# Kernel optimization log

Hardware: AMD Instinct MI355X
Metric: run time of the kernel (lower is better)

Reference implementation:

```python
import jax, jax.numpy as jnp
import numpy as np


def entmax15(scores, axis):
    """Exact entmax-1.5 (Peters & Martins 2019), sort-based threshold."""
    s = jnp.moveaxis(scores, axis, -1)
    s = (s - jnp.max(s, axis=-1, keepdims=True)) / 2.0
    d = s.shape[-1]
    srt = jnp.sort(s, axis=-1)[..., ::-1]  # descending
    rho = jnp.arange(1, d + 1, dtype=s.dtype)
    mean = jnp.cumsum(srt, axis=-1) / rho
    mean_sq = jnp.cumsum(srt * srt, axis=-1) / rho
    ss = rho * (mean_sq - mean * mean)
    delta = (1.0 - ss) / rho
    tau = mean - jnp.sqrt(jnp.clip(delta, 0.0, None))
    support = jnp.sum((tau <= srt).astype(jnp.int32), axis=-1)  # support size k*
    tau_star = jnp.take_along_axis(tau, (support - 1)[..., None], axis=-1)
    p = jnp.square(jnp.clip(s - tau_star, 0.0, None))
    return jnp.moveaxis(p, -1, axis)


def setup_inputs() -> dict:
    key = jax.random.key(0)
    k0, k1, k2 = jax.random.split(key, 3)
    B, S, H, A = 64, 2048, 512, 128
    lstm_output = jax.random.normal(k0, (B, S, H), dtype=jnp.float32)
    W1 = jax.random.normal(k1, (H, A), dtype=jnp.float32) * (1.0 / np.sqrt(H))
    b1 = jnp.zeros((A,), dtype=jnp.float32)
    W2 = jax.random.normal(k2, (A, 1), dtype=jnp.float32) * (1.0 / np.sqrt(A))
    b2 = jnp.zeros((1,), dtype=jnp.float32)
    return {"lstm_output": lstm_output, "W1": W1, "b1": b1, "W2": W2, "b2": b2}


def reference(lstm_output, W1, b1, W2, b2):
    # score MLP: Linear -> tanh -> Linear, squeeze(-1)
    h = jnp.tanh(lstm_output @ W1 + b1)            # [B, S, A]
    scores = (h @ W2)[..., 0] + b2[0]              # [B, S]
    weights = entmax15(scores, axis=1)             # sparse weights over seq dim
    context = jnp.einsum('bsh,bs->bh', lstm_output, weights)  # [B, H]
    return (context, weights)
```

## Files before the change

kernel.cpp:

```cpp
#include <hip/hip_runtime.h>
#include <math.h>

#define BB 64
#define SS 2048
#define HH 512
#define AA 128
#define MM (BB*SS)

typedef __attribute__((ext_vector_type(8)))  short short8;
typedef __attribute__((ext_vector_type(16))) float f32x16;

__device__ inline unsigned short f2bf_rne(float f) {
    unsigned u = __float_as_uint(f);
    unsigned r = (u + 0x7fff + ((u >> 16) & 1)) >> 16;
    return (unsigned short)r;
}
__device__ inline float bf2f(unsigned short h) {
    return __uint_as_float(((unsigned)h) << 16);
}
__device__ inline float fast_tanh(float x) {
    float t = __expf(2.0f * x);
    return 1.0f - 2.0f * __builtin_amdgcn_rcpf(t + 1.0f);
}

__global__ __launch_bounds__(256) void prep_w1t(
    const float* __restrict__ W1, unsigned short* __restrict__ W1Th,
    unsigned short* __restrict__ W1Tl)
{
    int idx = blockIdx.x * 256 + threadIdx.x;
    int n = idx & 127, k = idx >> 7;
    float v = W1[k * AA + n];
    unsigned short h = f2bf_rne(v);
    W1Th[n * HH + k] = h;
    W1Tl[n * HH + k] = f2bf_rne(v - bf2f(h));
}

__global__ __launch_bounds__(256, 2) void score_mfma(
    const float* __restrict__ X,
    const unsigned short* __restrict__ W1Th,
    const unsigned short* __restrict__ W1Tl,
    const float* __restrict__ b1, const float* __restrict__ W2,
    const float* __restrict__ b2, float* __restrict__ scores)
{
    __shared__ unsigned short B_lds[2][2][4][AA][8];

    const int tid  = threadIdx.x;
    const int wave = tid >> 6;
    const int lane = tid & 63;
    const int l31  = lane & 31;
    const int half = lane >> 5;
    const int m0   = blockIdx.x * 256;

    int sb_hilo[4], sb_g[4], sb_n[4];
    #pragma unroll
    for (int i = 0; i < 4; i++) {
        int c = tid + 256 * i;
        sb_hilo[i] = c >> 9;
        sb_g[i]    = (c >> 7) & 3;
        sb_n[i]    = c & 127;
    }

    const float* aptr0 = X + (size_t)(m0 + wave * 64      + l31) * HH + half * 8;
    const float* aptr1 = X + (size_t)(m0 + wave * 64 + 32 + l31) * HH + half * 8;

    f32x16 acc[2][4];
    #pragma unroll
    for (int mt = 0; mt < 2; mt++)
        #pragma unroll
        for (int nt = 0; nt < 4; nt++)
            #pragma unroll
            for (int j = 0; j < 16; j++) acc[mt][nt][j] = 0.f;

    short8 breg[4];
    float4 apre[2][2][2];

    #pragma unroll
    for (int i = 0; i < 4; i++) {
        const unsigned short* src = sb_hilo[i] ? W1Tl : W1Th;
        breg[i] = *(const short8*)(src + (size_t)sb_n[i] * HH + sb_g[i] * 8);
    }
    #pragma unroll
    for (int s = 0; s < 2; s++) {
        apre[0][s][0] = *(const float4*)(aptr0 + s * 16);
        apre[0][s][1] = *(const float4*)(aptr0 + s * 16 + 4);
        apre[1][s][0] = *(const float4*)(aptr1 + s * 16);
        apre[1][s][1] = *(const float4*)(aptr1 + s * 16 + 4);
    }
    #pragma unroll
    for (int i = 0; i < 4; i++)
        *(short8*)&B_lds[0][sb_hilo[i]][sb_g[i]][sb_n[i]][0] = breg[i];
    __syncthreads();

    for (int it = 0; it < 16; it++) {
        const int cur = it & 1;

        if (it < 15) {
            #pragma unroll
            for (int i = 0; i < 4; i++) {
                const unsigned short* src = sb_hilo[i] ? W1Tl : W1Th;
                breg[i] = *(const short8*)(src + (size_t)sb_n[i] * HH
                                           + (it + 1) * 32 + sb_g[i] * 8);
            }
        }

        short8 ah[2][2], al[2][2];
        #pragma unroll
        for (int mt = 0; mt < 2; mt++)
            #pragma unroll
            for (int s = 0; s < 2; s++) {
                float fs[8];
                *(float4*)&fs[0] = apre[mt][s][0];
                *(float4*)&fs[4] = apre[mt][s][1];
                #pragma unroll
                for (int j = 0; j < 8; j++) {
                    unsigned short h = f2bf_rne(fs[j]);
                    ah[mt][s][j] = (short)h;
                    float r = fs[j] - bf2f(h);
                    al[mt][s][j] = (short)(__float_as_uint(r) >> 16);
                }
            }

        if (it < 15) {
            #pragma unroll
            for (int s = 0; s < 2; s++) {
                apre[0][s][0] = *(const float4*)(aptr0 + (it + 1) * 32 + s * 16);
                apre[0][s][1] = *(const float4*)(aptr0 + (it + 1) * 32 + s * 16 + 4);
                apre[1][s][0] = *(const float4*)(aptr1 + (it + 1) * 32 + s * 16);
                apre[1][s][1] = *(const float4*)(aptr1 + (it + 1) * 32 + s * 16 + 4);
            }
        }

        #pragma unroll
        for (int s = 0; s < 2; s++) {
            const int gr = s * 2 + half;
            #pragma unroll
            for (int nt = 0; nt < 4; nt++) {
                short8 bh = *(const short8*)&B_lds[cur][0][gr][nt * 32 + l31][0];
                short8 bl = *(const short8*)&B_lds[cur][1][gr][nt * 32 + l31][0];
                acc[0][nt] = __builtin_amdgcn_mfma_f32_32x32x16_bf16(ah[0][s], bh, acc[0][nt], 0, 0, 0);
                acc[0][nt] = __builtin_amdgcn_mfma_f32_32x32x16_bf16(ah[0][s], bl, acc[0][nt], 0, 0, 0);
                acc[0][nt] = __builtin_amdgcn_mfma_f32_32x32x16_bf16(al[0][s], bh, acc[0][nt], 0, 0, 0);
                acc[1][nt] = __builtin_amdgcn_mfma_f32_32x32x16_bf16(ah[1][s], bh, acc[1][nt], 0, 0, 0);
                acc[1][nt] = __builtin_amdgcn_mfma_f32_32x32x16_bf16(ah[1][s], bl, acc[1][nt], 0, 0, 0);
                acc[1][nt] = __builtin_amdgcn_mfma_f32_32x32x16_bf16(al[1][s], bh, acc[1][nt], 0, 0, 0);
            }
        }

        if (it < 15) {
            #pragma unroll
            for (int i = 0; i < 4; i++)
                *(short8*)&B_lds[cur ^ 1][sb_hilo[i]][sb_g[i]][sb_n[i]][0] = breg[i];
        }
        __syncthreads();
    }

    const float bb2 = b2[0];
    #pragma unroll
    for (int mt = 0; mt < 2; mt++) {
        float part[16];
        #pragma unroll
        for (int r = 0; r < 16; r++) part[r] = 0.f;
        #pragma unroll
        for (int nt = 0; nt < 4; nt++) {
            int n = nt * 32 + l31;
            float bias = b1[n];
            float w2   = W2[n];
            #pragma unroll
            for (int r = 0; r < 16; r++)
                part[r] += fast_tanh(acc[mt][nt][r] + bias) * w2;
        }
        #pragma unroll
        for (int off = 16; off > 0; off >>= 1)
            #pragma unroll
            for (int r = 0; r < 16; r++)
                part[r] += __shfl_xor(part[r], off);
        if (l31 == 0) {
            #pragma unroll
            for (int r = 0; r < 16; r++) {
                int row = (r & 3) + 8 * (r >> 2) + 4 * half;
                scores[m0 + wave * 64 + mt * 32 + row] = part[r] + bb2;
            }
        }
    }
}

__global__ __launch_bounds__(256) void entmax_bisect(
    const float* __restrict__ scores, float* __restrict__ weights)
{
    __shared__ float red[4];
    const int t = threadIdx.x, b = blockIdx.x;
    const int wv = t >> 6, ln = t & 63;
    const float* row = scores + (size_t)b * SS;

    float v[8];
    #pragma unroll
    for (int i = 0; i < 8; i++) v[i] = row[t + 256 * i];

    float mx = v[0];
    #pragma unroll
    for (int i = 1; i < 8; i++) mx = fmaxf(mx, v[i]);
    #pragma unroll
    for (int off = 32; off > 0; off >>= 1) mx = fmaxf(mx, __shfl_xor(mx, off));
    if (ln == 0) red[wv] = mx;
    __syncthreads();
    mx = fmaxf(fmaxf(red[0], red[1]), fmaxf(red[2], red[3]));

    #pragma unroll
    for (int i = 0; i < 8; i++) v[i] = (v[i] - mx) * 0.5f;

    float lo = -1.0f, hi = 0.0f;
    for (int it = 0; it < 32; it++) {
        float tm = 0.5f * (lo + hi);
        float s = 0.f;
        #pragma unroll
        for (int i = 0; i < 8; i++) {
            float d = fmaxf(v[i] - tm, 0.f);
            s = fmaf(d, d, s);
        }
        #pragma unroll
        for (int off = 32; off > 0; off >>= 1) s += __shfl_xor(s, off);
        __syncthreads();
        if (ln == 0) red[wv] = s;
        __syncthreads();
        s = red[0] + red[1] + red[2] + red[3];
        if (s >= 1.0f) lo = tm; else hi = tm;
    }
    float tau = 0.5f * (lo + hi);

    #pragma unroll
    for (int i = 0; i < 8; i++) {
        float d = fmaxf(v[i] - tau, 0.f);
        weights[(size_t)b * SS + t + 256 * i] = d * d;
    }
}

__global__ __launch_bounds__(256) void context_kernel(
    const float* __restrict__ X, const float* __restrict__ weights,
    float* __restrict__ ctx)
{
    const int b = blockIdx.y;
    const int chunk = blockIdx.x;
    const int tid = threadIdx.x;
    const float* wrow  = weights + (size_t)b * SS + chunk * 64;
    const float* xbase = X + ((size_t)b * SS + (size_t)chunk * 64) * HH;
    float acc0 = 0.f, acc1 = 0.f;
    bool any = false;
    for (int s = 0; s < 64; s++) {
        float w = wrow[s];
        if (w != 0.f) {
            any = true;
            float2 x = *(const float2*)(xbase + (size_t)s * HH + 2 * tid);
            acc0 = fmaf(x.x, w, acc0);
            acc1 = fmaf(x.y, w, acc1);
        }
    }
    if (any) {
        atomicAdd(&ctx[b * HH + 2 * tid],     acc0);
        atomicAdd(&ctx[b * HH + 2 * tid + 1], acc1);
    }
}

extern "C" void kernel_launch(void* const* d_in, const int* in_sizes, int n_in,
                              void* d_out, int out_size, void* d_ws, size_t ws_size,
                              hipStream_t stream) {
    const float* X  = (const float*)d_in[0];
    const float* W1 = (const float*)d_in[1];
    const float* b1 = (const float*)d_in[2];
    const float* W2 = (const float*)d_in[3];
    const float* b2 = (const float*)d_in[4];

    float* out     = (float*)d_out;
    float* ctx     = out;
    float* weights = out + BB * HH;
    float* scores  = weights;

    unsigned short* W1Th = (unsigned short*)d_ws;
    unsigned short* W1Tl = W1Th + (size_t)AA * HH;

    hipMemsetAsync(ctx, 0, (size_t)BB * HH * sizeof(float), stream);
    prep_w1t<<<dim3(256), 256, 0, stream>>>(W1, W1Th, W1Tl);
    score_mfma<<<dim3(MM / 256), 256, 0, stream>>>(X, W1Th, W1Tl, b1, W2, b2, scores);
    entmax_bisect<<<dim3(BB), 256, 0, stream>>>(scores, weights);
    context_kernel<<<dim3(32, BB), 256, 0, stream>>>(X, weights, ctx);
}
```

Measured before the change: 404.4 us.

## Prepack W1 in MFMA fragment layout, Newton entmax, sparse-index context gather

```diff
diff --git a/kernel.cpp b/kernel.cpp
--- a/kernel.cpp
+++ b/kernel.cpp
@@ -24,26 +24,28 @@
 }
 
 __global__ __launch_bounds__(256) void prep_w1t(
-    const float* __restrict__ W1, unsigned short* __restrict__ W1Th,
-    unsigned short* __restrict__ W1Tl)
-{
-    int idx = blockIdx.x * 256 + threadIdx.x;
-    int n = idx & 127, k = idx >> 7;
+    const float* __restrict__ W1, unsigned short* __restrict__ PB)
+{
+    int id = blockIdx.x * 256 + threadIdx.x;
+    int n = id & 127, k = id >> 7;
     float v = W1[k * AA + n];
     unsigned short h = f2bf_rne(v);
-    W1Th[n * HH + k] = h;
-    W1Tl[n * HH + k] = f2bf_rne(v - bf2f(h));
+    unsigned short l = f2bf_rne(v - bf2f(h));
+    int it = k >> 5, r = k & 31;
+    int s = r >> 4, half = (r >> 3) & 1, j = r & 7;
+    int lane = half * 32 + (n & 31);
+    int nt = n >> 5;
+    size_t off = ((size_t)(((it * 2 + s) * 4 + nt) * 2) * 64 + lane) * 8 + j;
+    PB[off]       = h;
+    PB[off + 512] = l;
 }
 
 __global__ __launch_bounds__(256, 2) void score_mfma(
     const float* __restrict__ X,
-    const unsigned short* __restrict__ W1Th,
-    const unsigned short* __restrict__ W1Tl,
+    const unsigned short* __restrict__ PB,
     const float* __restrict__ b1, const float* __restrict__ W2,
     const float* __restrict__ b2, float* __restrict__ scores)
 {
-    __shared__ unsigned short B_lds[2][2][4][AA][8];
-
     const int tid  = threadIdx.x;
     const int wave = tid >> 6;
     const int lane = tid & 63;
@@ -51,17 +53,9 @@
     const int half = lane >> 5;
     const int m0   = blockIdx.x * 256;
 
-    int sb_hilo[4], sb_g[4], sb_n[4];
-    #pragma unroll
-    for (int i = 0; i < 4; i++) {
-        int c = tid + 256 * i;
-        sb_hilo[i] = c >> 9;
-        sb_g[i]    = (c >> 7) & 3;
-        sb_n[i]    = c & 127;
-    }
-
     const float* aptr0 = X + (size_t)(m0 + wave * 64      + l31) * HH + half * 8;
     const float* aptr1 = X + (size_t)(m0 + wave * 64 + 32 + l31) * HH + half * 8;
+    const unsigned short* pbl = PB + lane * 8;
 
     f32x16 acc[2][4];
     #pragma unroll
@@ -71,14 +65,7 @@
             #pragma unroll
             for (int j = 0; j < 16; j++) acc[mt][nt][j] = 0.f;
 
-    short8 breg[4];
     float4 apre[2][2][2];
-
-    #pragma unroll
-    for (int i = 0; i < 4; i++) {
-        const unsigned short* src = sb_hilo[i] ? W1Tl : W1Th;
-        breg[i] = *(const short8*)(src + (size_t)sb_n[i] * HH + sb_g[i] * 8);
-    }
     #pragma unroll
     for (int s = 0; s < 2; s++) {
         apre[0][s][0] = *(const float4*)(aptr0 + s * 16);
@@ -86,21 +73,15 @@
         apre[1][s][0] = *(const float4*)(aptr1 + s * 16);
         apre[1][s][1] = *(const float4*)(aptr1 + s * 16 + 4);
     }
-    #pragma unroll
-    for (int i = 0; i < 4; i++)
-        *(short8*)&B_lds[0][sb_hilo[i]][sb_g[i]][sb_n[i]][0] = breg[i];
-    __syncthreads();
-
+
+    #pragma unroll 1
     for (int it = 0; it < 16; it++) {
-        const int cur = it & 1;
-
-        if (it < 15) {
-            #pragma unroll
-            for (int i = 0; i < 4; i++) {
-                const unsigned short* src = sb_hilo[i] ? W1Tl : W1Th;
-                breg[i] = *(const short8*)(src + (size_t)sb_n[i] * HH
-                                           + (it + 1) * 32 + sb_g[i] * 8);
-            }
+        short8 bh[4], bl[4];
+        #pragma unroll
+        for (int nt = 0; nt < 4; nt++) {
+            const unsigned short* p = pbl + (size_t)((it * 2 + 0) * 4 + nt) * 1024;
+            bh[nt] = *(const short8*)(p);
+            bl[nt] = *(const short8*)(p + 512);
         }
 
         short8 ah[2][2], al[2][2];
@@ -120,6 +101,23 @@
                 }
             }
 
+        #pragma unroll
+        for (int nt = 0; nt < 4; nt++) {
+            acc[0][nt] = __builtin_amdgcn_mfma_f32_32x32x16_bf16(ah[0][0], bh[nt], acc[0][nt], 0, 0, 0);
+            acc[0][nt] = __builtin_amdgcn_mfma_f32_32x32x16_bf16(ah[0][0], bl[nt], acc[0][nt], 0, 0, 0);
+            acc[0][nt] = __builtin_amdgcn_mfma_f32_32x32x16_bf16(al[0][0], bh[nt], acc[0][nt], 0, 0, 0);
+            acc[1][nt] = __builtin_amdgcn_mfma_f32_32x32x16_bf16(ah[1][0], bh[nt], acc[1][nt], 0, 0, 0);
+            acc[1][nt] = __builtin_amdgcn_mfma_f32_32x32x16_bf16(ah[1][0], bl[nt], acc[1][nt], 0, 0, 0);
+            acc[1][nt] = __builtin_amdgcn_mfma_f32_32x32x16_bf16(al[1][0], bh[nt], acc[1][nt], 0, 0, 0);
+        }
+
+        #pragma unroll
+        for (int nt = 0; nt < 4; nt++) {
+            const unsigned short* p = pbl + (size_t)((it * 2 + 1) * 4 + nt) * 1024;
+            bh[nt] = *(const short8*)(p);
+            bl[nt] = *(const short8*)(p + 512);
+        }
+
         if (it < 15) {
             #pragma unroll
             for (int s = 0; s < 2; s++) {
@@ -131,27 +129,14 @@
         }
 
         #pragma unroll
-        for (int s = 0; s < 2; s++) {
-            const int gr = s * 2 + half;
-            #pragma unroll
-            for (int nt = 0; nt < 4; nt++) {
-                short8 bh = *(const short8*)&B_lds[cur][0][gr][nt * 32 + l31][0];
-                short8 bl = *(const short8*)&B_lds[cur][1][gr][nt * 32 + l31][0];
-                acc[0][nt] = __builtin_amdgcn_mfma_f32_32x32x16_bf16(ah[0][s], bh, acc[0][nt], 0, 0, 0);
-                acc[0][nt] = __builtin_amdgcn_mfma_f32_32x32x16_bf16(ah[0][s], bl, acc[0][nt], 0, 0, 0);
-                acc[0][nt] = __builtin_amdgcn_mfma_f32_32x32x16_bf16(al[0][s], bh, acc[0][nt], 0, 0, 0);
-                acc[1][nt] = __builtin_amdgcn_mfma_f32_32x32x16_bf16(ah[1][s], bh, acc[1][nt], 0, 0, 0);
-                acc[1][nt] = __builtin_amdgcn_mfma_f32_32x32x16_bf16(ah[1][s], bl, acc[1][nt], 0, 0, 0);
-                acc[1][nt] = __builtin_amdgcn_mfma_f32_32x32x16_bf16(al[1][s], bh, acc[1][nt], 0, 0, 0);
-            }
-        }
-
-        if (it < 15) {
-            #pragma unroll
-            for (int i = 0; i < 4; i++)
-                *(short8*)&B_lds[cur ^ 1][sb_hilo[i]][sb_g[i]][sb_n[i]][0] = breg[i];
-        }
-        __syncthreads();
+        for (int nt = 0; nt < 4; nt++) {
+            acc[0][nt] = __builtin_amdgcn_mfma_f32_32x32x16_bf16(ah[0][1], bh[nt], acc[0][nt], 0, 0, 0);
+            acc[0][nt] = __builtin_amdgcn_mfma_f32_32x32x16_bf16(ah[0][1], bl[nt], acc[0][nt], 0, 0, 0);
+            acc[0][nt] = __builtin_amdgcn_mfma_f32_32x32x16_bf16(al[0][1], bh[nt], acc[0][nt], 0, 0, 0);
+            acc[1][nt] = __builtin_amdgcn_mfma_f32_32x32x16_bf16(ah[1][1], bh[nt], acc[1][nt], 0, 0, 0);
+            acc[1][nt] = __builtin_amdgcn_mfma_f32_32x32x16_bf16(ah[1][1], bl[nt], acc[1][nt], 0, 0, 0);
+            acc[1][nt] = __builtin_amdgcn_mfma_f32_32x32x16_bf16(al[1][1], bh[nt], acc[1][nt], 0, 0, 0);
+        }
     }
 
     const float bb2 = b2[0];
@@ -184,10 +169,12 @@
     }
 }
 
-__global__ __launch_bounds__(256) void entmax_bisect(
-    const float* __restrict__ scores, float* __restrict__ weights)
-{
-    __shared__ float red[4];
+__global__ __launch_bounds__(256) void entmax_newton(
+    const float* __restrict__ scores, float* __restrict__ weights,
+    unsigned short* __restrict__ nzidx, int* __restrict__ nzcount)
+{
+    __shared__ float red[4][2];
+    __shared__ int cnt;
     const int t = threadIdx.x, b = blockIdx.x;
     const int wv = t >> 6, ln = t & 63;
     const float* row = scores + (size_t)b * SS;
@@ -201,60 +188,69 @@
     for (int i = 1; i < 8; i++) mx = fmaxf(mx, v[i]);
     #pragma unroll
     for (int off = 32; off > 0; off >>= 1) mx = fmaxf(mx, __shfl_xor(mx, off));
-    if (ln == 0) red[wv] = mx;
+    if (t == 0) cnt = 0;
+    if (ln == 0) red[wv][0] = mx;
     __syncthreads();
-    mx = fmaxf(fmaxf(red[0], red[1]), fmaxf(red[2], red[3]));
+    mx = fmaxf(fmaxf(red[0][0], red[1][0]), fmaxf(red[2][0], red[3][0]));
 
     #pragma unroll
     for (int i = 0; i < 8; i++) v[i] = (v[i] - mx) * 0.5f;
 
-    float lo = -1.0f, hi = 0.0f;
-    for (int it = 0; it < 32; it++) {
-        float tm = 0.5f * (lo + hi);
-        float s = 0.f;
+    float tau = -1.0f;
+    for (int nit = 0; nit < 14; ++nit) {
+        float s1 = 0.f, s2 = 0.f;
         #pragma unroll
         for (int i = 0; i < 8; i++) {
-            float d = fmaxf(v[i] - tm, 0.f);
-            s = fmaf(d, d, s);
-        }
-        #pragma unroll
-        for (int off = 32; off > 0; off >>= 1) s += __shfl_xor(s, off);
+            float d = fmaxf(v[i] - tau, 0.f);
+            s1 += d;
+            s2 = fmaf(d, d, s2);
+        }
+        #pragma unroll
+        for (int off = 32; off > 0; off >>= 1) {
+            s1 += __shfl_xor(s1, off);
+            s2 += __shfl_xor(s2, off);
+        }
         __syncthreads();
-        if (ln == 0) red[wv] = s;
+        if (ln == 0) { red[wv][0] = s1; red[wv][1] = s2; }
         __syncthreads();
-        s = red[0] + red[1] + red[2] + red[3];
-        if (s >= 1.0f) lo = tm; else hi = tm;
-    }
-    float tau = 0.5f * (lo + hi);
+        s1 = red[0][0] + red[1][0] + red[2][0] + red[3][0];
+        s2 = red[0][1] + red[1][1] + red[2][1] + red[3][1];
+        tau += (s2 - 1.0f) / (2.0f * s1);
+    }
 
     #pragma unroll
     for (int i = 0; i < 8; i++) {
         float d = fmaxf(v[i] - tau, 0.f);
         weights[(size_t)b * SS + t + 256 * i] = d * d;
-    }
+        if (d > 0.f) {
+            int p = atomicAdd(&cnt, 1);
+            nzidx[(size_t)b * SS + p] = (unsigned short)(t + 256 * i);
+        }
+    }
+    __syncthreads();
+    if (t == 0) nzcount[b] = cnt;
 }
 
 __global__ __launch_bounds__(256) void context_kernel(
     const float* __restrict__ X, const float* __restrict__ weights,
+    const unsigned short* __restrict__ nzidx, const int* __restrict__ nzcount,
     float* __restrict__ ctx)
 {
     const int b = blockIdx.y;
-    const int chunk = blockIdx.x;
+    const int c = blockIdx.x;
     const int tid = threadIdx.x;
-    const float* wrow  = weights + (size_t)b * SS + chunk * 64;
-    const float* xbase = X + ((size_t)b * SS + (size_t)chunk * 64) * HH;
+    const int n = nzcount[b];
+    const unsigned short* ib = nzidx + (size_t)b * SS;
+    const float* wrow = weights + (size_t)b * SS;
     float acc0 = 0.f, acc1 = 0.f;
-    bool any = false;
-    for (int s = 0; s < 64; s++) {
+    for (int e = c; e < n; e += 32) {
+        int s = ib[e];
         float w = wrow[s];
-        if (w != 0.f) {
-            any = true;
-            float2 x = *(const float2*)(xbase + (size_t)s * HH + 2 * tid);
-            acc0 = fmaf(x.x, w, acc0);
-            acc1 = fmaf(x.y, w, acc1);
-        }
-    }
-    if (any) {
+        float2 x = *(const float2*)(X + ((size_t)b * SS + s) * HH + 2 * tid);
+        acc0 = fmaf(x.x, w, acc0);
+        acc1 = fmaf(x.y, w, acc1);
+    }
+    if (n > c) {
         atomicAdd(&ctx[b * HH + 2 * tid],     acc0);
         atomicAdd(&ctx[b * HH + 2 * tid + 1], acc1);
     }
@@ -274,12 +270,13 @@
     float* weights = out + BB * HH;
     float* scores  = weights;
 
-    unsigned short* W1Th = (unsigned short*)d_ws;
-    unsigned short* W1Tl = W1Th + (size_t)AA * HH;
+    unsigned short* PB      = (unsigned short*)d_ws;
+    unsigned short* nzidx   = PB + (size_t)AA * HH * 2;
+    int*            nzcount = (int*)(nzidx + (size_t)BB * SS);
 
     hipMemsetAsync(ctx, 0, (size_t)BB * HH * sizeof(float), stream);
-    prep_w1t<<<dim3(256), 256, 0, stream>>>(W1, W1Th, W1Tl);
-    score_mfma<<<dim3(MM / 256), 256, 0, stream>>>(X, W1Th, W1Tl, b1, W2, b2, scores);
-    entmax_bisect<<<dim3(BB), 256, 0, stream>>>(scores, weights);
-    context_kernel<<<dim3(32, BB), 256, 0, stream>>>(X, weights, ctx);
-}
+    prep_w1t<<<dim3(256), 256, 0, stream>>>(W1, PB);
+    score_mfma<<<dim3(MM / 256), 256, 0, stream>>>(X, PB, b1, W2, b2, scores);
+    entmax_newton<<<dim3(BB), 256, 0, stream>>>(scores, weights, nzidx, nzcount);
+    context_kernel<<<dim3(32, BB), 256, 0, stream>>>(X, weights, nzidx, nzcount, ctx);
+}
```

After: 401.5 us. No clear change (-0.7%).
